# Performance work log

Measured on AMD Instinct MI355X. Metric: run time of the kernel, lower is better.

The kernel has to match this reference:

```python
import jax, jax.numpy as jnp
import numpy as np

B, N, C, H = 8, 128, 256, 8
HS = C // H
SCALE = HS ** -0.5
EPS = 1e-5


def layernorm(x, w, b):
    mu = jnp.mean(x, axis=-1, keepdims=True)
    var = jnp.var(x, axis=-1, keepdims=True)
    return (x - mu) * jax.lax.rsqrt(var + EPS) * w + b


def setup_inputs() -> dict:
    key = jax.random.key(0)
    ks = jax.random.split(key, 12)
    inp = {
        "joint_feature": jax.random.normal(ks[0], (B, N, C), jnp.float32),
        "relation_feature": jax.random.normal(ks[1], (B, N, N, C), jnp.float32),
        "conn_feature": jax.random.uniform(ks[2], (B, N, N), jnp.float32),
        # LayerNorm params
        "ln1_w": jnp.ones((C,), jnp.float32), "ln1_b": jnp.zeros((C,), jnp.float32),
        "ln2_w": jnp.ones((C,), jnp.float32), "ln2_b": jnp.zeros((C,), jnp.float32),
        "ln3_w": jnp.ones((C,), jnp.float32), "ln3_b": jnp.zeros((C,), jnp.float32),
        # Attention params (qkv_bias=False)
        "qkv_w": 0.02 * jax.random.normal(ks[3], (3 * C, C), jnp.float32),
        "rconv_w": 0.02 * jax.random.normal(ks[4], (H, C), jnp.float32),
        "proj_w": 0.02 * jax.random.normal(ks[5], (C, C), jnp.float32),
        "proj_b": jnp.zeros((C,), jnp.float32),
        # Mlp params (hidden_features == dim in this Block)
        "fc1_w": 0.02 * jax.random.normal(ks[6], (C, C), jnp.float32),
        "fc1_b": jnp.zeros((C,), jnp.float32),
        "fc2_w": 0.02 * jax.random.normal(ks[7], (C, C), jnp.float32),
        "fc2_b": jnp.zeros((C,), jnp.float32),
    }
    return inp


def reference(joint_feature, relation_feature, conn_feature,
              ln1_w, ln1_b, ln2_w, ln2_b, ln3_w, ln3_b,
              qkv_w, rconv_w, proj_w, proj_b,
              fc1_w, fc1_b, fc2_w, fc2_b):
    # --- Attention branch ---
    jn = layernorm(joint_feature, ln1_w, ln1_b)          # [B,N,C]
    rn = layernorm(relation_feature, ln2_w, ln2_b)       # [B,N,N,C]
    qkv = jn @ qkv_w.T                                   # [B,N,3C]
    qkv = qkv.reshape(B, N, 3, H, HS)
    q = jnp.transpose(qkv[:, :, 0], (0, 2, 1, 3))        # [B,H,N,HS]
    k = jnp.transpose(qkv[:, :, 1], (0, 2, 1, 3))
    v = jnp.transpose(qkv[:, :, 2], (0, 2, 1, 3))
    attn_J = jnp.einsum('bhnd,bhmd->bhnm', q, k)         # [B,H,N,N]
    attn_R = jnp.einsum('bnmc,hc->bhnm', rn, rconv_w)    # [B,H,N,N]
    attn = (attn_J + attn_R) * conn_feature[:, None] * SCALE
    attn = jax.nn.softmax(attn, axis=-1)
    x = jnp.einsum('bhnm,bhmd->bnhd', attn, v).reshape(B, N, C)
    x = x @ proj_w.T + proj_b
    joint = joint_feature + x
    # --- MLP branch (hidden = dim, exact GELU as torch nn.GELU) ---
    h = layernorm(joint, ln3_w, ln3_b)
    h = jax.nn.gelu(h @ fc1_w.T + fc1_b, approximate=False)
    h = h @ fc2_w.T + fc2_b
    return joint + h
```

## Files before the change

kernel.cpp:

```cpp
#include <hip/hip_runtime.h>
#include <hip/hip_bf16.h>

#define Bb 8
#define Nn 128
#define Cc 256
#define SCALE 0.1767766952966369f
#define EPS 1e-5f

typedef short v8s __attribute__((ext_vector_type(8)));
typedef short v4s __attribute__((ext_vector_type(4)));
typedef float v4f __attribute__((ext_vector_type(4)));
using bf16_t = __hip_bfloat16;

__device__ inline float bf2f(bf16_t h){ return __bfloat162float(h); }
__device__ inline short f2bfbits(float f){
    unsigned int u = __float_as_uint(f);
    u += 0x7fff + ((u >> 16) & 1u);
    return (short)(u >> 16);
}

__device__ inline float rscatter8(const float (&S)[8], int l){
    bool b0 = l & 1, b1 = l & 2, b2 = l & 4;
    float t[4];
#pragma unroll
    for (int k = 0; k < 4; k++){
        float keep = b0 ? S[k+4] : S[k];
        float give = b0 ? S[k]   : S[k+4];
        t[k] = keep + __shfl_xor(give, 1);
    }
    float u[2];
#pragma unroll
    for (int k = 0; k < 2; k++){
        float keep = b1 ? t[k+2] : t[k];
        float give = b1 ? t[k]   : t[k+2];
        u[k] = keep + __shfl_xor(give, 2);
    }
    float r;
    {
        float keep = b2 ? u[1] : u[0];
        float give = b2 ? u[0] : u[1];
        r = keep + __shfl_xor(give, 4);
    }
    r += __shfl_xor(r, 8);
    r += __shfl_xor(r, 16);
    return r;
}

__global__ __launch_bounds__(256) void relnorm_kernel(
        const float* __restrict__ rel,
        const float* __restrict__ ln2w,
        const float* __restrict__ ln2b,
        const float* __restrict__ rconv,
        float* __restrict__ R)
{
    const int lane = threadIdx.x & 63;
    const int hl = lane & 31;
    const int c0 = hl * 8;

    float w2[8][8];
    float Tp[8] = {0,0,0,0,0,0,0,0};
    float Bp[8] = {0,0,0,0,0,0,0,0};
#pragma unroll
    for (int j = 0; j < 8; j++){
        float lw = ln2w[c0 + j];
        float lb = ln2b[c0 + j];
#pragma unroll
        for (int hh = 0; hh < 8; hh++){
            float rc = rconv[hh * Cc + c0 + j];
            w2[j][hh] = lw * rc;
            Tp[hh] += w2[j][hh];
            Bp[hh] = fmaf(lb, rc, Bp[hh]);
        }
    }
    const float Th = rscatter8(Tp, hl);
    const float Bh = rscatter8(Bp, hl);
    const int h = (hl & 1) * 4 + ((hl >> 1) & 1) * 2 + ((hl >> 2) & 1);

    const int hw = (blockIdx.x * blockDim.x + threadIdx.x) >> 5;
    const int hwStride = (gridDim.x * blockDim.x) >> 5;
    const int totalRows = Bb * Nn * Nn;

    for (int row = hw; row < totalRows; row += hwStride){
        const float* rp = rel + (size_t)row * Cc + c0;
        float4 xa = *(const float4*)(rp);
        float4 xb = *(const float4*)(rp + 4);
        float x[8] = { xa.x, xa.y, xa.z, xa.w, xb.x, xb.y, xb.z, xb.w };
        float sum = 0.f, sq = 0.f;
        float S[8] = {0,0,0,0,0,0,0,0};
#pragma unroll
        for (int j = 0; j < 8; j++){
            float xv = x[j];
            sum += xv;
            sq = fmaf(xv, xv, sq);
#pragma unroll
            for (int hh = 0; hh < 8; hh++)
                S[hh] = fmaf(xv, w2[j][hh], S[hh]);
        }
#pragma unroll
        for (int o = 1; o <= 16; o <<= 1){
            sum += __shfl_xor(sum, o);
            sq  += __shfl_xor(sq,  o);
        }
        float mu = sum * (1.f / 256.f);
        float rstd = rsqrtf(sq * (1.f / 256.f) - mu * mu + EPS);
        float Sh = rscatter8(S, hl);
        if (hl < 8)
            R[(size_t)row * 8 + h] = rstd * (Sh - mu * Th) + Bh;
    }
}

__global__ __launch_bounds__(256) void ln_kernel(
        const float* __restrict__ x, const float* __restrict__ w,
        const float* __restrict__ bv, short* __restrict__ y)
{
    const int lane = threadIdx.x & 63;
    const int row = blockIdx.x * 4 + (threadIdx.x >> 6);
    const int c0 = lane * 4;
    float4 xv4 = *(const float4*)(x + (size_t)row * Cc + c0);
    float xv[4] = { xv4.x, xv4.y, xv4.z, xv4.w };
    float sum = xv[0] + xv[1] + xv[2] + xv[3];
    float sq = fmaf(xv[0], xv[0], fmaf(xv[1], xv[1], fmaf(xv[2], xv[2], xv[3]*xv[3])));
#pragma unroll
    for (int o = 1; o <= 32; o <<= 1){
        sum += __shfl_xor(sum, o);
        sq  += __shfl_xor(sq,  o);
    }
    float mu = sum * (1.f / 256.f);
    float rstd = rsqrtf(sq * (1.f / 256.f) - mu * mu + EPS);
    float4 wv = *(const float4*)(w + c0);
    float4 bb = *(const float4*)(bv + c0);
    v4s o;
    o[0] = f2bfbits((xv[0]-mu)*rstd*wv.x + bb.x);
    o[1] = f2bfbits((xv[1]-mu)*rstd*wv.y + bb.y);
    o[2] = f2bfbits((xv[2]-mu)*rstd*wv.z + bb.z);
    o[3] = f2bfbits((xv[3]-mu)*rstd*wv.w + bb.w);
    *(v4s*)(y + (size_t)row * Cc + c0) = o;
}

template<int NTOT, int EPI>
__global__ __launch_bounds__(256) void gemm_kernel(
        const bf16_t* __restrict__ A, const float* __restrict__ W,
        const float* __restrict__ bias, const float* __restrict__ res,
        void* __restrict__ out)
{
    const int lane = threadIdx.x & 63;
    const int wv = threadIdx.x >> 6;
    const int mtile = blockIdx.x * 16;
    const int ntile = blockIdx.y * 64 + wv * 16;
    const int mi = lane & 15, q = lane >> 4;
    const bf16_t* ap = A + (size_t)(mtile + mi) * Cc + q * 8;
    const float* wp = W + (size_t)(ntile + mi) * Cc + q * 8;
    v4f acc = {0.f, 0.f, 0.f, 0.f};
#pragma unroll
    for (int kk = 0; kk < 8; kk++){
        v8s af = *(const v8s*)(ap + kk * 32);
        float4 w0 = *(const float4*)(wp + kk * 32);
        float4 w1 = *(const float4*)(wp + kk * 32 + 4);
        v8s bf;
        bf[0]=f2bfbits(w0.x); bf[1]=f2bfbits(w0.y); bf[2]=f2bfbits(w0.z); bf[3]=f2bfbits(w0.w);
        bf[4]=f2bfbits(w1.x); bf[5]=f2bfbits(w1.y); bf[6]=f2bfbits(w1.z); bf[7]=f2bfbits(w1.w);
        acc = __builtin_amdgcn_mfma_f32_16x16x32_bf16(af, bf, acc, 0, 0, 0);
    }
    const int n = ntile + mi;
    float bia = (EPI > 0) ? bias[n] : 0.f;
#pragma unroll
    for (int r = 0; r < 4; r++){
        int m = mtile + q * 4 + r;
        float v = acc[r] + bia;
        if (EPI == 0){
            ((short*)out)[(size_t)m * NTOT + n] = f2bfbits(v);
        } else if (EPI == 1){
            v += res[(size_t)m * Cc + n];
            ((float*)out)[(size_t)m * Cc + n] = v;
        } else if (EPI == 2){
            v = 0.5f * v * (1.f + erff(v * 0.70710678118654752f));
            ((short*)out)[(size_t)m * Cc + n] = f2bfbits(v);
        } else {
            v += res[(size_t)m * Cc + n];
            ((float*)out)[(size_t)m * Cc + n] = v;
        }
    }
}

__global__ __launch_bounds__(256) void attn_kernel(
        const bf16_t* __restrict__ qkv,
        const float* __restrict__ R,
        const float* __restrict__ conn,
        short* __restrict__ xatt)
{
    const int bid = blockIdx.x;
    const int b = bid >> 5;
    const int h = (bid >> 2) & 7;
    const int nq = bid & 3;
    __shared__ float k_s[128 * 36];
    __shared__ float v_s[128 * 32];
    __shared__ float q_s[32 * 33];
    __shared__ float p_s[32 * 132];
    const int t = threadIdx.x;
    const bf16_t* qkvb = qkv + (size_t)b * Nn * 768;

#pragma unroll
    for (int i = 0; i < 16; i++){
        int idx = t + i * 256;
        int m = idx >> 5, d = idx & 31;
        k_s[m * 36 + d] = bf2f(qkvb[m * 768 + 256 + h * 32 + d]);
        v_s[m * 32 + d] = bf2f(qkvb[m * 768 + 512 + h * 32 + d]);
    }
#pragma unroll
    for (int i = 0; i < 4; i++){
        int idx = t + i * 256;
        int nl = idx >> 5, d = idx & 31;
        q_s[nl * 33 + d] = bf2f(qkvb[(nq * 32 + nl) * 768 + h * 32 + d]);
    }
    __syncthreads();

    const int nl = t >> 3, tg = t & 7;
    const int n = nq * 32 + nl;
    float qr[32];
#pragma unroll
    for (int d = 0; d < 32; d++) qr[d] = q_s[nl * 33 + d];
    const float* Rrow = R + ((size_t)(b * Nn + n) * Nn) * 8 + h;
    const float* crow = conn + (size_t)(b * Nn + n) * Nn;

    float s[16];
#pragma unroll
    for (int i = 0; i < 16; i++){
        int m = tg + 8 * i;
        float acc = 0.f;
#pragma unroll
        for (int g = 0; g < 8; g++){
            float4 kv = *(const float4*)&k_s[m * 36 + g * 4];
            acc = fmaf(qr[g*4+0], kv.x, acc);
            acc = fmaf(qr[g*4+1], kv.y, acc);
            acc = fmaf(qr[g*4+2], kv.z, acc);
            acc = fmaf(qr[g*4+3], kv.w, acc);
        }
        s[i] = (acc + Rrow[(size_t)m * 8]) * crow[m] * SCALE;
    }
    float mx = s[0];
#pragma unroll
    for (int i = 1; i < 16; i++) mx = fmaxf(mx, s[i]);
    mx = fmaxf(mx, __shfl_xor(mx, 1));
    mx = fmaxf(mx, __shfl_xor(mx, 2));
    mx = fmaxf(mx, __shfl_xor(mx, 4));
    float lsum = 0.f;
#pragma unroll
    for (int i = 0; i < 16; i++){ s[i] = expf(s[i] - mx); lsum += s[i]; }
    lsum += __shfl_xor(lsum, 1);
    lsum += __shfl_xor(lsum, 2);
    lsum += __shfl_xor(lsum, 4);
    float inv = 1.f / lsum;
#pragma unroll
    for (int i = 0; i < 16; i++)
        p_s[nl * 132 + tg + 8 * i] = s[i] * inv;
    __syncthreads();

    const int d0 = tg * 4;
    float a0 = 0.f, a1 = 0.f, a2 = 0.f, a3 = 0.f;
    for (int m = 0; m < 128; m++){
        float p = p_s[nl * 132 + m];
        float4 vv = *(const float4*)&v_s[m * 32 + d0];
        a0 = fmaf(p, vv.x, a0);
        a1 = fmaf(p, vv.y, a1);
        a2 = fmaf(p, vv.z, a2);
        a3 = fmaf(p, vv.w, a3);
    }
    v4s o4; o4[0]=f2bfbits(a0); o4[1]=f2bfbits(a1); o4[2]=f2bfbits(a2); o4[3]=f2bfbits(a3);
    *(v4s*)(xatt + (size_t)(b * Nn + n) * Cc + h * 32 + d0) = o4;
}

extern "C" void kernel_launch(void* const* d_in, const int* in_sizes, int n_in,
                              void* d_out, int out_size, void* d_ws, size_t ws_size,
                              hipStream_t stream)
{
    const float* joint  = (const float*)d_in[0];
    const float* rel    = (const float*)d_in[1];
    const float* conn   = (const float*)d_in[2];
    const float* ln1w   = (const float*)d_in[3];
    const float* ln1b   = (const float*)d_in[4];
    const float* ln2w   = (const float*)d_in[5];
    const float* ln2b   = (const float*)d_in[6];
    const float* ln3w   = (const float*)d_in[7];
    const float* ln3b   = (const float*)d_in[8];
    const float* qkvw   = (const float*)d_in[9];
    const float* rconv  = (const float*)d_in[10];
    const float* projw  = (const float*)d_in[11];
    const float* projb  = (const float*)d_in[12];
    const float* fc1w   = (const float*)d_in[13];
    const float* fc1b   = (const float*)d_in[14];
    const float* fc2w   = (const float*)d_in[15];
    const float* fc2b   = (const float*)d_in[16];

    char* w = (char*)d_ws;
    float* Rf     = (float*)(w);
    short* qkvb   = (short*)(w + 4194304);
    short* jnb    = (short*)(w + 5767168);
    short* xattb  = (short*)(w + 6291456);
    float* joint2 = (float*)(w + 6815744);
    short* h1b    = (short*)(w + 7864320);
    short* h2b    = (short*)(w + 8388608);

    relnorm_kernel<<<dim3(2048), dim3(256), 0, stream>>>(rel, ln2w, ln2b, rconv, Rf);
    ln_kernel<<<dim3(256), dim3(256), 0, stream>>>(joint, ln1w, ln1b, jnb);
    gemm_kernel<768, 0><<<dim3(64, 12), dim3(256), 0, stream>>>(
        (const bf16_t*)jnb, qkvw, nullptr, nullptr, qkvb);
    attn_kernel<<<dim3(256), dim3(256), 0, stream>>>(
        (const bf16_t*)qkvb, Rf, conn, xattb);
    gemm_kernel<256, 1><<<dim3(64, 4), dim3(256), 0, stream>>>(
        (const bf16_t*)xattb, projw, projb, joint, joint2);
    ln_kernel<<<dim3(256), dim3(256), 0, stream>>>(joint2, ln3w, ln3b, h1b);
    gemm_kernel<256, 2><<<dim3(64, 4), dim3(256), 0, stream>>>(
        (const bf16_t*)h1b, fc1w, fc1b, nullptr, h2b);
    gemm_kernel<256, 3><<<dim3(64, 4), dim3(256), 0, stream>>>(
        (const bf16_t*)h2b, fc2w, fc2b, joint2, (float*)d_out);
}
```

Baseline: 267.8 us.

## Fuse layernorms into GEMMs and co-schedule QKV with relation norm

Result: faster. 258.7 us (median of 2 runs) (-3.4%).

```diff
diff --git a/kernel.cpp b/kernel.cpp
--- a/kernel.cpp
+++ b/kernel.cpp
@@ -46,13 +46,90 @@
     return r;
 }
 
-__global__ __launch_bounds__(256) void relnorm_kernel(
+template<int NTOT, int EPI>
+__device__ __forceinline__ void lngemm_body(
+        const float* __restrict__ A, const float* __restrict__ lnw,
+        const float* __restrict__ lnb, const float* __restrict__ W,
+        const float* __restrict__ bias, short* __restrict__ out,
+        int mtile, int ntile0)
+{
+    __shared__ short a_s[16][264];
+    __shared__ float red[2][16][16];
+    const int t = threadIdx.x;
+    const int r = t >> 4, j = t & 15;
+    const float* rowp = A + (size_t)(mtile + r) * Cc + j * 16;
+    float x[16];
+#pragma unroll
+    for (int i = 0; i < 4; i++){
+        float4 v = *(const float4*)(rowp + i * 4);
+        x[i*4+0]=v.x; x[i*4+1]=v.y; x[i*4+2]=v.z; x[i*4+3]=v.w;
+    }
+    float s1 = 0.f, s2 = 0.f;
+#pragma unroll
+    for (int i = 0; i < 16; i++){ s1 += x[i]; s2 = fmaf(x[i], x[i], s2); }
+    red[0][r][j] = s1; red[1][r][j] = s2;
+    __syncthreads();
+    float t1 = 0.f, t2 = 0.f;
+#pragma unroll
+    for (int i = 0; i < 16; i++){ t1 += red[0][r][i]; t2 += red[1][r][i]; }
+    const float mu = t1 * (1.f/256.f);
+    const float rstd = rsqrtf(t2 * (1.f/256.f) - mu*mu + EPS);
+    short pk[16];
+#pragma unroll
+    for (int i = 0; i < 4; i++){
+        float4 wv4 = *(const float4*)(lnw + j*16 + i*4);
+        float4 bv4 = *(const float4*)(lnb + j*16 + i*4);
+        pk[i*4+0] = f2bfbits((x[i*4+0]-mu)*rstd*wv4.x + bv4.x);
+        pk[i*4+1] = f2bfbits((x[i*4+1]-mu)*rstd*wv4.y + bv4.y);
+        pk[i*4+2] = f2bfbits((x[i*4+2]-mu)*rstd*wv4.z + bv4.z);
+        pk[i*4+3] = f2bfbits((x[i*4+3]-mu)*rstd*wv4.w + bv4.w);
+    }
+    *(v8s*)&a_s[r][j*16]     = *(v8s*)&pk[0];
+    *(v8s*)&a_s[r][j*16 + 8] = *(v8s*)&pk[8];
+    __syncthreads();
+
+    const int lane = t & 63;
+    const int wv = t >> 6;
+    const int ntile = ntile0 + wv * 16;
+    const int mi = lane & 15, q = lane >> 4;
+    const short* alds = &a_s[mi][q * 8];
+    const float* wp = W + (size_t)(ntile + mi) * Cc + q * 8;
+    v4f acc = {0.f, 0.f, 0.f, 0.f};
+#pragma unroll
+    for (int kk = 0; kk < 8; kk++){
+        v8s af = *(const v8s*)(alds + kk * 32);
+        float4 w0 = *(const float4*)(wp + kk * 32);
+        float4 w1 = *(const float4*)(wp + kk * 32 + 4);
+        v8s bf;
+        bf[0]=f2bfbits(w0.x); bf[1]=f2bfbits(w0.y); bf[2]=f2bfbits(w0.z); bf[3]=f2bfbits(w0.w);
+        bf[4]=f2bfbits(w1.x); bf[5]=f2bfbits(w1.y); bf[6]=f2bfbits(w1.z); bf[7]=f2bfbits(w1.w);
+        acc = __builtin_amdgcn_mfma_f32_16x16x32_bf16(af, bf, acc, 0, 0, 0);
+    }
+    const int n = ntile + mi;
+    const float bia = (EPI == 2) ? bias[n] : 0.f;
+#pragma unroll
+    for (int rr = 0; rr < 4; rr++){
+        int m = mtile + q * 4 + rr;
+        float v = acc[rr] + bia;
+        if (EPI == 2) v = 0.5f * v * (1.f + erff(v * 0.70710678118654752f));
+        out[(size_t)m * NTOT + n] = f2bfbits(v);
+    }
+}
+
+__global__ __launch_bounds__(256) void mega1_kernel(
         const float* __restrict__ rel,
-        const float* __restrict__ ln2w,
-        const float* __restrict__ ln2b,
-        const float* __restrict__ rconv,
-        float* __restrict__ R)
-{
+        const float* __restrict__ ln2w, const float* __restrict__ ln2b,
+        const float* __restrict__ rconv, short* __restrict__ R,
+        const float* __restrict__ joint,
+        const float* __restrict__ ln1w, const float* __restrict__ ln1b,
+        const float* __restrict__ qkvw, short* __restrict__ qkvb)
+{
+    if (blockIdx.x >= 2048){
+        const int bx = blockIdx.x - 2048;
+        lngemm_body<768, 0>(joint, ln1w, ln1b, qkvw, nullptr, qkvb,
+                            (bx & 63) * 16, (bx >> 6) * 64);
+        return;
+    }
     const int lane = threadIdx.x & 63;
     const int hl = lane & 31;
     const int c0 = hl * 8;
@@ -76,8 +153,8 @@
     const float Bh = rscatter8(Bp, hl);
     const int h = (hl & 1) * 4 + ((hl >> 1) & 1) * 2 + ((hl >> 2) & 1);
 
-    const int hw = (blockIdx.x * blockDim.x + threadIdx.x) >> 5;
-    const int hwStride = (gridDim.x * blockDim.x) >> 5;
+    const int hw = (blockIdx.x * 256 + threadIdx.x) >> 5;
+    const int hwStride = (2048 * 256) >> 5;
     const int totalRows = Bb * Nn * Nn;
 
     for (int row = hw; row < totalRows; row += hwStride){
@@ -105,43 +182,15 @@
         float rstd = rsqrtf(sq * (1.f / 256.f) - mu * mu + EPS);
         float Sh = rscatter8(S, hl);
         if (hl < 8)
-            R[(size_t)row * 8 + h] = rstd * (Sh - mu * Th) + Bh;
-    }
-}
-
-__global__ __launch_bounds__(256) void ln_kernel(
-        const float* __restrict__ x, const float* __restrict__ w,
-        const float* __restrict__ bv, short* __restrict__ y)
-{
-    const int lane = threadIdx.x & 63;
-    const int row = blockIdx.x * 4 + (threadIdx.x >> 6);
-    const int c0 = lane * 4;
-    float4 xv4 = *(const float4*)(x + (size_t)row * Cc + c0);
-    float xv[4] = { xv4.x, xv4.y, xv4.z, xv4.w };
-    float sum = xv[0] + xv[1] + xv[2] + xv[3];
-    float sq = fmaf(xv[0], xv[0], fmaf(xv[1], xv[1], fmaf(xv[2], xv[2], xv[3]*xv[3])));
-#pragma unroll
-    for (int o = 1; o <= 32; o <<= 1){
-        sum += __shfl_xor(sum, o);
-        sq  += __shfl_xor(sq,  o);
-    }
-    float mu = sum * (1.f / 256.f);
-    float rstd = rsqrtf(sq * (1.f / 256.f) - mu * mu + EPS);
-    float4 wv = *(const float4*)(w + c0);
-    float4 bb = *(const float4*)(bv + c0);
-    v4s o;
-    o[0] = f2bfbits((xv[0]-mu)*rstd*wv.x + bb.x);
-    o[1] = f2bfbits((xv[1]-mu)*rstd*wv.y + bb.y);
-    o[2] = f2bfbits((xv[2]-mu)*rstd*wv.z + bb.z);
-    o[3] = f2bfbits((xv[3]-mu)*rstd*wv.w + bb.w);
-    *(v4s*)(y + (size_t)row * Cc + c0) = o;
-}
-
-template<int NTOT, int EPI>
+            R[(size_t)row * 8 + h] = f2bfbits(rstd * (Sh - mu * Th) + Bh);
+    }
+}
+
+template<int EPI>
 __global__ __launch_bounds__(256) void gemm_kernel(
         const bf16_t* __restrict__ A, const float* __restrict__ W,
         const float* __restrict__ bias, const float* __restrict__ res,
-        void* __restrict__ out)
+        float* __restrict__ out)
 {
     const int lane = threadIdx.x & 63;
     const int wv = threadIdx.x >> 6;
@@ -162,29 +211,28 @@
         acc = __builtin_amdgcn_mfma_f32_16x16x32_bf16(af, bf, acc, 0, 0, 0);
     }
     const int n = ntile + mi;
-    float bia = (EPI > 0) ? bias[n] : 0.f;
+    const float bia = bias[n];
 #pragma unroll
     for (int r = 0; r < 4; r++){
         int m = mtile + q * 4 + r;
-        float v = acc[r] + bia;
-        if (EPI == 0){
-            ((short*)out)[(size_t)m * NTOT + n] = f2bfbits(v);
-        } else if (EPI == 1){
-            v += res[(size_t)m * Cc + n];
-            ((float*)out)[(size_t)m * Cc + n] = v;
-        } else if (EPI == 2){
-            v = 0.5f * v * (1.f + erff(v * 0.70710678118654752f));
-            ((short*)out)[(size_t)m * Cc + n] = f2bfbits(v);
-        } else {
-            v += res[(size_t)m * Cc + n];
-            ((float*)out)[(size_t)m * Cc + n] = v;
-        }
-    }
+        float v = acc[r] + bia + res[(size_t)m * Cc + n];
+        out[(size_t)m * Cc + n] = v;
+    }
+}
+
+__global__ __launch_bounds__(256) void fc1_kernel(
+        const float* __restrict__ joint2,
+        const float* __restrict__ ln3w, const float* __restrict__ ln3b,
+        const float* __restrict__ fc1w, const float* __restrict__ fc1b,
+        short* __restrict__ h2)
+{
+    lngemm_body<256, 2>(joint2, ln3w, ln3b, fc1w, fc1b, h2,
+                        blockIdx.x * 16, blockIdx.y * 64);
 }
 
 __global__ __launch_bounds__(256) void attn_kernel(
         const bf16_t* __restrict__ qkv,
-        const float* __restrict__ R,
+        const bf16_t* __restrict__ R,
         const float* __restrict__ conn,
         short* __restrict__ xatt)
 {
@@ -219,7 +267,7 @@
     float qr[32];
 #pragma unroll
     for (int d = 0; d < 32; d++) qr[d] = q_s[nl * 33 + d];
-    const float* Rrow = R + ((size_t)(b * Nn + n) * Nn) * 8 + h;
+    const bf16_t* Rrow = R + ((size_t)(b * Nn + n) * Nn) * 8 + h;
     const float* crow = conn + (size_t)(b * Nn + n) * Nn;
 
     float s[16];
@@ -235,7 +283,7 @@
             acc = fmaf(qr[g*4+2], kv.z, acc);
             acc = fmaf(qr[g*4+3], kv.w, acc);
         }
-        s[i] = (acc + Rrow[(size_t)m * 8]) * crow[m] * SCALE;
+        s[i] = (acc + bf2f(Rrow[(size_t)m * 8])) * crow[m] * SCALE;
     }
     float mx = s[0];
 #pragma unroll
@@ -292,25 +340,20 @@
     const float* fc2b   = (const float*)d_in[16];
 
     char* w = (char*)d_ws;
-    float* Rf     = (float*)(w);
-    short* qkvb   = (short*)(w + 4194304);
-    short* jnb    = (short*)(w + 5767168);
-    short* xattb  = (short*)(w + 6291456);
-    float* joint2 = (float*)(w + 6815744);
-    short* h1b    = (short*)(w + 7864320);
-    short* h2b    = (short*)(w + 8388608);
-
-    relnorm_kernel<<<dim3(2048), dim3(256), 0, stream>>>(rel, ln2w, ln2b, rconv, Rf);
-    ln_kernel<<<dim3(256), dim3(256), 0, stream>>>(joint, ln1w, ln1b, jnb);
-    gemm_kernel<768, 0><<<dim3(64, 12), dim3(256), 0, stream>>>(
-        (const bf16_t*)jnb, qkvw, nullptr, nullptr, qkvb);
+    short* Rb     = (short*)(w);
+    short* qkvb   = (short*)(w + 2097152);
+    short* xattb  = (short*)(w + 3670016);
+    float* joint2 = (float*)(w + 4194304);
+    short* h2b    = (short*)(w + 5242880);
+
+    mega1_kernel<<<dim3(2816), dim3(256), 0, stream>>>(
+        rel, ln2w, ln2b, rconv, Rb, joint, ln1w, ln1b, qkvw, qkvb);
     attn_kernel<<<dim3(256), dim3(256), 0, stream>>>(
-        (const bf16_t*)qkvb, Rf, conn, xattb);
-    gemm_kernel<256, 1><<<dim3(64, 4), dim3(256), 0, stream>>>(
+        (const bf16_t*)qkvb, (const bf16_t*)Rb, conn, xattb);
+    gemm_kernel<1><<<dim3(64, 4), dim3(256), 0, stream>>>(
         (const bf16_t*)xattb, projw, projb, joint, joint2);
-    ln_kernel<<<dim3(256), dim3(256), 0, stream>>>(joint2, ln3w, ln3b, h1b);
-    gemm_kernel<256, 2><<<dim3(64, 4), dim3(256), 0, stream>>>(
-        (const bf16_t*)h1b, fc1w, fc1b, nullptr, h2b);
-    gemm_kernel<256, 3><<<dim3(64, 4), dim3(256), 0, stream>>>(
+    fc1_kernel<<<dim3(64, 4), dim3(256), 0, stream>>>(
+        joint2, ln3w, ln3b, fc1w, fc1b, h2b);
+    gemm_kernel<3><<<dim3(64, 4), dim3(256), 0, stream>>>(
         (const bf16_t*)h2b, fc2w, fc2b, joint2, (float*)d_out);
 }
```
